# Performance work log

Hardware: AMD Instinct MI355X
Metric: run time of the kernel (lower is better)

The kernel has to match this reference:

```python
import jax, jax.numpy as jnp
import numpy as np

DIM = 512
HEADS = 8
HEAD_DIM = DIM // HEADS  # 64
NUM_ENC = 32             # num_encoding_channels
ENC_RANGE = 1.0
OFFSETS = (0, 512, 2560) # B=2 point clouds, num_points=(512, 2048)
B = len(OFFSETS) - 1
M = 2048                 # max num_points -> padded length
TOTAL = OFFSETS[-1]      # 2560 total points
ENC_IN = NUM_ENC * 3 + 3 # 99 (concat_input=True)


def setup_inputs() -> dict:
    key = jax.random.key(0)
    ks = jax.random.split(key, 6)
    return {
        "features": jax.random.normal(ks[0], (TOTAL, DIM), jnp.float32),
        "coordinates": jax.random.uniform(ks[1], (TOTAL, 3), jnp.float32),
        "qkv_w": jax.random.normal(ks[2], (3 * DIM, DIM), jnp.float32) * (DIM ** -0.5),
        "proj_w": jax.random.normal(ks[3], (DIM, DIM), jnp.float32) * (DIM ** -0.5),
        "proj_b": jnp.zeros((DIM,), jnp.float32),
        "pos_w": jax.random.normal(ks[4], (HEAD_DIM, ENC_IN), jnp.float32) * (ENC_IN ** -0.5),
        "pos_b": jnp.zeros((HEAD_DIM,), jnp.float32),
        "offsets": jnp.array(OFFSETS, jnp.int32),
    }


def reference(features, coordinates, qkv_w, proj_w, proj_b, pos_w, pos_b, offsets):
    # ragged -> padded index math (replaces cat_to_pad / pad_to_cat Python loops)
    pt = jnp.arange(TOTAL)
    b_idx = jnp.searchsorted(offsets, pt, side='right') - 1   # batch id per point
    w_idx = pt - offsets[b_idx]                                # within-batch position
    num_points = offsets[1:] - offsets[:-1]                    # [B]

    # SinusoidalEncoding(num_channels=32, concat_input=True) + Linear -> head_dim
    half = NUM_ENC // 2
    freqs = (2.0 ** jnp.arange(half, dtype=jnp.float32)) * jnp.pi / ENC_RANGE
    sc = coordinates[..., None] * freqs                        # [T, 3, half]
    enc = jnp.concatenate([jnp.sin(sc), jnp.cos(sc)], -1).reshape(TOTAL, 3 * NUM_ENC)
    enc = jnp.concatenate([enc, coordinates], -1)              # [T, 99]
    pos = enc @ pos_w.T + pos_b                                # [T, head_dim]

    feat_pad = jnp.zeros((B, M, DIM), features.dtype).at[b_idx, w_idx].set(features)
    pos_pad = jnp.zeros((B, M, HEAD_DIM), pos.dtype).at[b_idx, w_idx].set(pos)

    # offset_to_mask: mask[b, :, :offsets[b], :offsets[b]] = -inf (cumulative offsets!)
    r = jnp.arange(M)
    off_b = offsets[:-1]                                       # [B]
    blocked = (r[None, :, None] < off_b[:, None, None]) & (r[None, None, :] < off_b[:, None, None])
    mask = jnp.where(blocked, -jnp.inf, 0.0)[:, None]          # [B, 1, M, M]

    # attention
    qkv = (feat_pad @ qkv_w.T).reshape(B, M, 3, HEADS, HEAD_DIM)
    qkv = jnp.transpose(qkv, (2, 0, 3, 1, 4))                  # [3, B, H, M, hd]
    q, k, v = qkv[0], qkv[1], qkv[2]
    q = q + pos_pad[:, None]                                   # broadcast over heads
    k = k + pos_pad[:, None]
    scale = HEAD_DIM ** -0.5
    scores = jnp.einsum('bhqd,bhkd->bhqk', q, k) * scale + mask
    attn = jax.nn.softmax(scores, axis=-1)
    y = jnp.einsum('bhqk,bhkd->bhqd', attn, v)                 # [B, H, M, hd]
    y = jnp.transpose(y, (0, 2, 1, 3)).reshape(B, M, DIM)
    y = y @ proj_w.T + proj_b

    # zero_out_points: x[b, num_points[b]:] = 0
    valid = r[None, :] < num_points[:, None]
    y = jnp.where(valid[..., None], y, 0.0)

    # pad_to_cat back to ragged [total_N, C]
    return y[b_idx, w_idx]
```

## Files before the change

### kernel.cpp

```cpp
#include <hip/hip_runtime.h>
#include <math.h>

#define TOTAL 2560
#define NEG_BIG (-1e30f)
#define LOG2E_8 0.18033688011112042f

typedef __bf16 bf16x8 __attribute__((ext_vector_type(8)));
typedef float f32x4 __attribute__((ext_vector_type(4)));
typedef unsigned short ushort8v __attribute__((ext_vector_type(8)));
typedef unsigned short ushort4v __attribute__((ext_vector_type(4)));

__device__ inline unsigned short f2bf(float f) {
    unsigned u = __builtin_bit_cast(unsigned, f);
    u += 0x7fff + ((u >> 16) & 1);
    return (unsigned short)(u >> 16);
}

__device__ inline void gload16(const void* g, void* l) {
    __builtin_amdgcn_global_load_lds(
        (const __attribute__((address_space(1))) void*)g,
        (__attribute__((address_space(3))) void*)l, 16, 0, 0);
}

__global__ __launch_bounds__(256) void pos_kernel(
    const float* __restrict__ coords,
    const float* __restrict__ pos_w,
    const float* __restrict__ pos_b,
    float* __restrict__ pos_out)
{
    __shared__ float enc[4][100];
    const int wv   = threadIdx.x >> 6;
    const int lane = threadIdx.x & 63;
    const int p = blockIdx.x * 4 + wv;
    const float c0 = coords[p * 3 + 0];
    const float c1 = coords[p * 3 + 1];
    const float c2 = coords[p * 3 + 2];
    for (int i = lane; i < 99; i += 64) {
        float v;
        if (i < 96) {
            const int d = i >> 5;
            const int j = i & 31;
            const float cv = (d == 0) ? c0 : ((d == 1) ? c1 : c2);
            const float freq = exp2f((float)(j & 15)) * 3.14159265358979323846f;
            const float sc = cv * freq;
            v = (j < 16) ? sinf(sc) : cosf(sc);
        } else {
            v = (i == 96) ? c0 : ((i == 97) ? c1 : c2);
        }
        enc[wv][i] = v;
    }
    float acc = pos_b[lane];
    const float* w = pos_w + lane * 99;
    for (int i = 0; i < 99; ++i) acc = fmaf(enc[wv][i], w[i], acc);
    pos_out[p * 64 + lane] = acc;
}

__global__ __launch_bounds__(256) void cast_kernel(
    const float* __restrict__ f,  const float* __restrict__ qw, const float* __restrict__ pw,
    unsigned short* __restrict__ fb, unsigned short* __restrict__ qwb, unsigned short* __restrict__ pwb)
{
    const int s = blockIdx.x * 256 + threadIdx.x;
    const float* src; unsigned short* dst; int ls;
    if (s < 163840)      { src = f;  dst = fb;  ls = s; }
    else if (s < 262144) { src = qw; dst = qwb; ls = s - 163840; }
    else                 { src = pw; dst = pwb; ls = s - 262144; }
    const float4 x0 = *(const float4*)(src + ls * 8);
    const float4 x1 = *(const float4*)(src + ls * 8 + 4);
    ushort8v o;
    o[0] = f2bf(x0.x); o[1] = f2bf(x0.y); o[2] = f2bf(x0.z); o[3] = f2bf(x0.w);
    o[4] = f2bf(x1.x); o[5] = f2bf(x1.y); o[6] = f2bf(x1.z); o[7] = f2bf(x1.w);
    *(ushort8v*)(dst + ls * 8) = o;
}

__global__ __launch_bounds__(256) void qkv_mfma_kernel(
    const unsigned short* __restrict__ A,
    const unsigned short* __restrict__ Bm,
    const float* __restrict__ pos,
    unsigned short* __restrict__ q_ws,
    unsigned short* __restrict__ k_ws,
    unsigned short* __restrict__ vt_ws)
{
    __shared__ unsigned short Abuf[2][64 * 64];
    __shared__ unsigned short Bbuf[2][64 * 64];
    const int m0 = blockIdx.x * 64;
    const int n0 = blockIdx.y * 64;
    const int t = threadIdx.x;
    const int w = t >> 6, lane = t & 63;
    const int wr = w >> 1, wc = w & 1;
    const int c = lane & 15, g = lane >> 4;

    auto STAGE = [&](int kt, int cur) {
#pragma unroll
        for (int i = 0; i < 2; ++i) {
            const int off = w * 2048 + i * 1024;
            const int ba  = off + lane * 16;
            const int row = ba >> 7;
            const int slot = (ba & 127) >> 4;
            gload16(A  + (m0 + row) * 512 + kt * 64 + ((slot ^ (row & 7)) * 8),
                    (char*)&Abuf[cur][0] + off);
            gload16(Bm + (n0 + row) * 512 + kt * 64 + ((slot ^ (row & 7)) * 8),
                    (char*)&Bbuf[cur][0] + off);
        }
    };

    f32x4 acc[2][2];
#pragma unroll
    for (int mi = 0; mi < 2; ++mi)
#pragma unroll
        for (int ni = 0; ni < 2; ++ni) acc[mi][ni] = (f32x4){0.f, 0.f, 0.f, 0.f};

    STAGE(0, 0);
    int cur = 0;
    for (int kt = 0; kt < 8; ++kt) {
        __syncthreads();
        if (kt + 1 < 8) STAGE(kt + 1, cur ^ 1);
#pragma unroll
        for (int kk = 0; kk < 2; ++kk) {
            bf16x8 af[2], bfr[2];
#pragma unroll
            for (int mi = 0; mi < 2; ++mi) {
                const int row = wr * 32 + mi * 16 + c;
                af[mi] = *(const bf16x8*)&Abuf[cur][row * 64 + ((g + 4 * kk) ^ (row & 7)) * 8];
            }
#pragma unroll
            for (int ni = 0; ni < 2; ++ni) {
                const int row = wc * 32 + ni * 16 + c;
                bfr[ni] = *(const bf16x8*)&Bbuf[cur][row * 64 + ((g + 4 * kk) ^ (row & 7)) * 8];
            }
#pragma unroll
            for (int mi = 0; mi < 2; ++mi)
#pragma unroll
                for (int ni = 0; ni < 2; ++ni)
                    acc[mi][ni] = __builtin_amdgcn_mfma_f32_16x16x32_bf16(af[mi], bfr[ni], acc[mi][ni], 0, 0, 0);
        }
        cur ^= 1;
    }

    const int which = n0 >> 9;
    const int h = (n0 >> 6) & 7;
#pragma unroll
    for (int mi = 0; mi < 2; ++mi)
#pragma unroll
        for (int ni = 0; ni < 2; ++ni) {
            const int dd = wc * 32 + ni * 16 + c;
            const int p0 = m0 + wr * 32 + mi * 16 + 4 * g;
            if (which == 2) {
                ushort4v o4;
#pragma unroll
                for (int r = 0; r < 4; ++r) o4[r] = f2bf(acc[mi][ni][r]);
                *(ushort4v*)(vt_ws + (h * 64 + dd) * TOTAL + p0) = o4;
            } else {
#pragma unroll
                for (int r = 0; r < 4; ++r) {
                    const int p = p0 + r;
                    const float v = acc[mi][ni][r] + pos[p * 64 + dd];
                    const int idx = (h * TOTAL + p) * 64 + dd;
                    if (which == 0) q_ws[idx] = f2bf(v);
                    else            k_ws[idx] = f2bf(v);
                }
            }
        }
}

__global__ __launch_bounds__(256) void attn_kernel(
    const unsigned short* __restrict__ q_ws,
    const unsigned short* __restrict__ k_ws,
    const unsigned short* __restrict__ vt_ws,
    unsigned short* __restrict__ y)
{
    const int bx = blockIdx.x;
    int b, qt, h;
    if (bx < 64) { b = 0; h = bx >> 3; qt = bx & 7; }
    else         { b = 1; const int rr = bx - 64; h = rr >> 5; qt = rr & 31; }
    const int base = b ? 512 : 0;
    const int nkt  = b ? 16 : 4;
    const int kt0  = (b && qt < 8) ? 4 : 0;

    const int t    = threadIdx.x;
    const int w    = t >> 6;
    const int lane = t & 63;
    const int g    = lane >> 4;
    const int c    = lane & 15;

    __shared__ unsigned short Kbuf[2][128 * 64];
    __shared__ unsigned short Vbuf[2][64 * 128];
    __shared__ unsigned short P_lds[64][72];

    const unsigned short* Qrow = q_ws + ((h * TOTAL) + base + qt * 64 + 16 * w + c) * 64;
    const bf16x8 qa0 = *(const bf16x8*)(Qrow + 8 * g);
    const bf16x8 qa1 = *(const bf16x8*)(Qrow + 8 * g + 32);

    float m_old = NEG_BIG, l_old = 0.f;
    f32x4 o_acc[4];
#pragma unroll
    for (int n = 0; n < 4; ++n) o_acc[n] = (f32x4){0.f, 0.f, 0.f, 0.f};

    const unsigned short* Kg = k_ws + (h * TOTAL + base) * 64;
    const unsigned short* Vg = vt_ws + h * 64 * TOTAL + base;

    auto STAGE = [&](int kt, int cur) {
#pragma unroll
        for (int i = 0; i < 4; ++i) {
            const int off = w * 4096 + i * 1024;
            const int ba  = off + lane * 16;
            {
                const int row = ba >> 7, slot = (ba & 127) >> 4;
                gload16(Kg + (kt * 128 + row) * 64 + ((slot ^ (row & 7)) * 8),
                        (char*)&Kbuf[cur][0] + off);
            }
            {
                const int dd = ba >> 8, slot = (ba & 255) >> 4;
                gload16(Vg + dd * TOTAL + kt * 128 + ((slot ^ (dd & 7)) * 8),
                        (char*)&Vbuf[cur][0] + off);
            }
        }
    };

    STAGE(kt0, 0);
    int cur = 0;
    for (int kt = kt0; kt < nkt; ++kt) {
        __syncthreads();
        if (kt + 1 < nkt) STAGE(kt + 1, cur ^ 1);

        const unsigned short* Ksh = &Kbuf[cur][0];
        const unsigned short* Vsh = &Vbuf[cur][0];

        f32x4 s_acc[8];
#pragma unroll
        for (int n = 0; n < 8; ++n) {
            f32x4 acc = (f32x4){0.f, 0.f, 0.f, 0.f};
            const int row = 16 * n + c;
            const bf16x8 kb0 = *(const bf16x8*)&Ksh[row * 64 + ((g + 0) ^ (c & 7)) * 8];
            const bf16x8 kb1 = *(const bf16x8*)&Ksh[row * 64 + ((g + 4) ^ (c & 7)) * 8];
            acc = __builtin_amdgcn_mfma_f32_16x16x32_bf16(kb0, qa0, acc, 0, 0, 0);
            acc = __builtin_amdgcn_mfma_f32_16x16x32_bf16(kb1, qa1, acc, 0, 0, 0);
            s_acc[n] = acc;
        }

        float mx01, mx23;
        {
            f32x4 m4 = s_acc[0];
#pragma unroll
            for (int n = 1; n < 8; ++n) {
#pragma unroll
                for (int r = 0; r < 4; ++r) m4[r] = fmaxf(m4[r], s_acc[n][r]);
            }
            mx01 = fmaxf(m4[0], m4[1]); mx23 = fmaxf(m4[2], m4[3]);
        }
        float tm = fmaxf(mx01, mx23) * LOG2E_8;
        tm = fmaxf(tm, __shfl_xor(tm, 16));
        tm = fmaxf(tm, __shfl_xor(tm, 32));
        const float m_new = fmaxf(m_old, tm);
        const float corr = exp2f(m_old - m_new);
        float rs = 0.f;
#pragma unroll
        for (int n = 0; n < 8; ++n)
#pragma unroll
            for (int r = 0; r < 4; ++r) {
                const float pv = exp2f(fmaf(s_acc[n][r], LOG2E_8, -m_new));
                s_acc[n][r] = pv;
                rs += pv;
            }
        rs += __shfl_xor(rs, 16);
        rs += __shfl_xor(rs, 32);
        l_old = l_old * corr + rs;
        m_old = m_new;

        float corr_r[4];
#pragma unroll
        for (int r = 0; r < 4; ++r) corr_r[r] = __shfl(corr, 4 * g + r);
#pragma unroll
        for (int n = 0; n < 4; ++n)
#pragma unroll
            for (int r = 0; r < 4; ++r) o_acc[n][r] *= corr_r[r];

#pragma unroll
        for (int half = 0; half < 2; ++half) {
#pragma unroll
            for (int n = 0; n < 4; ++n) {
                ushort4v pk;
#pragma unroll
                for (int r = 0; r < 4; ++r) pk[r] = f2bf(s_acc[half * 4 + n][r]);
                *(ushort4v*)&P_lds[16 * w + c][16 * n + 4 * g] = pk;
            }
#pragma unroll
            for (int kk = 0; kk < 2; ++kk) {
                const bf16x8 pa = *(const bf16x8*)&P_lds[16 * w + c][8 * g + 32 * kk];
                const int vslot = (g + 4 * (half * 2 + kk)) ^ (c & 7);
#pragma unroll
                for (int n = 0; n < 4; ++n) {
                    const bf16x8 vb = *(const bf16x8*)&Vsh[(16 * n + c) * 128 + vslot * 8];
                    o_acc[n] = __builtin_amdgcn_mfma_f32_16x16x32_bf16(pa, vb, o_acc[n], 0, 0, 0);
                }
            }
        }
        cur ^= 1;
    }

    float inv_own;
    if (b == 0) {
        const float mn  = fmaxf(m_old, 0.f);
        const float ccf = exp2f(m_old - mn);
        const float l   = l_old * ccf + 1536.0f * exp2f(-mn);
        inv_own = ccf / l;
    } else {
        inv_own = 1.0f / l_old;
    }
    float inv_r[4];
#pragma unroll
    for (int r = 0; r < 4; ++r) inv_r[r] = __shfl(inv_own, 4 * g + r);
    unsigned short* yb = y + (base + qt * 64 + 16 * w) * 512 + h * 64;
#pragma unroll
    for (int n = 0; n < 4; ++n)
#pragma unroll
        for (int r = 0; r < 4; ++r)
            yb[(4 * g + r) * 512 + 16 * n + c] = f2bf(o_acc[n][r] * inv_r[r]);
}

__global__ __launch_bounds__(256) void proj_mfma_kernel(
    const unsigned short* __restrict__ A,
    const unsigned short* __restrict__ Bm,
    const float* __restrict__ bias,
    float* __restrict__ out)
{
    __shared__ unsigned short Abuf[2][64 * 64];
    __shared__ unsigned short Bbuf[2][64 * 64];
    const int m0 = blockIdx.x * 64;
    const int n0 = blockIdx.y * 64;
    const int t = threadIdx.x;
    const int w = t >> 6, lane = t & 63;
    const int wr = w >> 1, wc = w & 1;
    const int c = lane & 15, g = lane >> 4;

    auto STAGE = [&](int kt, int cur) {
#pragma unroll
        for (int i = 0; i < 2; ++i) {
            const int off = w * 2048 + i * 1024;
            const int ba  = off + lane * 16;
            const int row = ba >> 7;
            const int slot = (ba & 127) >> 4;
            gload16(A  + (m0 + row) * 512 + kt * 64 + ((slot ^ (row & 7)) * 8),
                    (char*)&Abuf[cur][0] + off);
            gload16(Bm + (n0 + row) * 512 + kt * 64 + ((slot ^ (row & 7)) * 8),
                    (char*)&Bbuf[cur][0] + off);
        }
    };

    f32x4 acc[2][2];
#pragma unroll
    for (int mi = 0; mi < 2; ++mi)
#pragma unroll
        for (int ni = 0; ni < 2; ++ni) acc[mi][ni] = (f32x4){0.f, 0.f, 0.f, 0.f};

    STAGE(0, 0);
    int cur = 0;
    for (int kt = 0; kt < 8; ++kt) {
        __syncthreads();
        if (kt + 1 < 8) STAGE(kt + 1, cur ^ 1);
#pragma unroll
        for (int kk = 0; kk < 2; ++kk) {
            bf16x8 af[2], bfr[2];
#pragma unroll
            for (int mi = 0; mi < 2; ++mi) {
                const int row = wr * 32 + mi * 16 + c;
                af[mi] = *(const bf16x8*)&Abuf[cur][row * 64 + ((g + 4 * kk) ^ (row & 7)) * 8];
            }
#pragma unroll
            for (int ni = 0; ni < 2; ++ni) {
                const int row = wc * 32 + ni * 16 + c;
                bfr[ni] = *(const bf16x8*)&Bbuf[cur][row * 64 + ((g + 4 * kk) ^ (row & 7)) * 8];
            }
#pragma unroll
            for (int mi = 0; mi < 2; ++mi)
#pragma unroll
                for (int ni = 0; ni < 2; ++ni)
                    acc[mi][ni] = __builtin_amdgcn_mfma_f32_16x16x32_bf16(af[mi], bfr[ni], acc[mi][ni], 0, 0, 0);
        }
        cur ^= 1;
    }

#pragma unroll
    for (int mi = 0; mi < 2; ++mi)
#pragma unroll
        for (int ni = 0; ni < 2; ++ni) {
            const int col = n0 + wc * 32 + ni * 16 + c;
            const float bv = bias[col];
#pragma unroll
            for (int r = 0; r < 4; ++r) {
                const int p = m0 + wr * 32 + mi * 16 + 4 * g + r;
                out[p * 512 + col] = acc[mi][ni][r] + bv;
            }
        }
}

extern "C" void kernel_launch(void* const* d_in, const int* in_sizes, int n_in,
                              void* d_out, int out_size, void* d_ws, size_t ws_size,
                              hipStream_t stream) {
    const float* features = (const float*)d_in[0];
    const float* coords   = (const float*)d_in[1];
    const float* qkv_w    = (const float*)d_in[2];
    const float* proj_w   = (const float*)d_in[3];
    const float* proj_b   = (const float*)d_in[4];
    const float* pos_w    = (const float*)d_in[5];
    const float* pos_b    = (const float*)d_in[6];
    float* out = (float*)d_out;

    float* pos_ws = (float*)d_ws;
    unsigned short* feat_bf  = (unsigned short*)(pos_ws + TOTAL * 64);
    unsigned short* qkvw_bf  = feat_bf + 2560 * 512;
    unsigned short* projw_bf = qkvw_bf + 1536 * 512;
    unsigned short* q_ws  = projw_bf + 512 * 512;
    unsigned short* k_ws  = q_ws  + 8 * TOTAL * 64;
    unsigned short* vt_ws = k_ws  + 8 * TOTAL * 64;
    unsigned short* y_bf  = vt_ws + 8 * TOTAL * 64;

    pos_kernel<<<dim3(TOTAL / 4), dim3(256), 0, stream>>>(coords, pos_w, pos_b, pos_ws);
    cast_kernel<<<dim3(1152), dim3(256), 0, stream>>>(
        features, qkv_w, proj_w, feat_bf, qkvw_bf, projw_bf);
    qkv_mfma_kernel<<<dim3(40, 24), dim3(256), 0, stream>>>(
        feat_bf, qkvw_bf, pos_ws, q_ws, k_ws, vt_ws);
    attn_kernel<<<dim3(320), dim3(256), 0, stream>>>(q_ws, k_ws, vt_ws, y_bf);
    proj_mfma_kernel<<<dim3(40, 8), dim3(256), 0, stream>>>(
        y_bf, projw_bf, proj_b, out);
}
```

Measured before the change: 71.49 us.

## Split attention KV range into two partials and combine, reading K/V directly from global

The attention kernel for the second batch is split along the key dimension into two halves, so 576 blocks launch instead of 320. Each half writes unnormalized fp32 partial outputs plus running max and sum, and a new combine kernel merges them and casts to bf16. The LDS double-buffered K/V staging is removed; K and V fragments are now loaded straight from global memory (L2) inside the MFMA loops. The aim is to fill more CUs on the mi355x, at the cost of an extra launch, fp32 partial traffic, and uncoalesced global loads in place of staged shared-memory loads.

```diff
diff --git a/kernel.cpp b/kernel.cpp
--- a/kernel.cpp
+++ b/kernel.cpp
@@ -162,19 +162,29 @@
         }
 }
 
-__global__ __launch_bounds__(256) void attn_kernel(
+__global__ __launch_bounds__(256) void attn_part_kernel(
     const unsigned short* __restrict__ q_ws,
     const unsigned short* __restrict__ k_ws,
     const unsigned short* __restrict__ vt_ws,
-    unsigned short* __restrict__ y)
+    float* __restrict__ o_part,
+    float2* __restrict__ ml2)
 {
     const int bx = blockIdx.x;
-    int b, qt, h;
-    if (bx < 64) { b = 0; h = bx >> 3; qt = bx & 7; }
-    else         { b = 1; const int rr = bx - 64; h = rr >> 5; qt = rr & 31; }
+    int b, qt, h, sp, t0, t1;
+    if (bx < 64) {
+        b = 0; h = bx >> 3; qt = bx & 7; sp = 0; t0 = 0; t1 = 4;
+    } else {
+        b = 1;
+        const int idx = bx - 64;
+        sp = idx >> 8;
+        const int rr = idx & 255;
+        h = rr >> 5; qt = rr & 31;
+        const int kt0 = (qt < 8) ? 4 : 0;
+        const int mid = (kt0 + 16) >> 1;
+        t0 = sp ? mid : kt0;
+        t1 = sp ? 16 : mid;
+    }
     const int base = b ? 512 : 0;
-    const int nkt  = b ? 16 : 4;
-    const int kt0  = (b && qt < 8) ? 4 : 0;
 
     const int t    = threadIdx.x;
     const int w    = t >> 6;
@@ -182,8 +192,6 @@
     const int g    = lane >> 4;
     const int c    = lane & 15;
 
-    __shared__ unsigned short Kbuf[2][128 * 64];
-    __shared__ unsigned short Vbuf[2][64 * 128];
     __shared__ unsigned short P_lds[64][72];
 
     const unsigned short* Qrow = q_ws + ((h * TOTAL) + base + qt * 64 + 16 * w + c) * 64;
@@ -198,40 +206,16 @@
     const unsigned short* Kg = k_ws + (h * TOTAL + base) * 64;
     const unsigned short* Vg = vt_ws + h * 64 * TOTAL + base;
 
-    auto STAGE = [&](int kt, int cur) {
-#pragma unroll
-        for (int i = 0; i < 4; ++i) {
-            const int off = w * 4096 + i * 1024;
-            const int ba  = off + lane * 16;
-            {
-                const int row = ba >> 7, slot = (ba & 127) >> 4;
-                gload16(Kg + (kt * 128 + row) * 64 + ((slot ^ (row & 7)) * 8),
-                        (char*)&Kbuf[cur][0] + off);
-            }
-            {
-                const int dd = ba >> 8, slot = (ba & 255) >> 4;
-                gload16(Vg + dd * TOTAL + kt * 128 + ((slot ^ (dd & 7)) * 8),
-                        (char*)&Vbuf[cur][0] + off);
-            }
-        }
-    };
-
-    STAGE(kt0, 0);
-    int cur = 0;
-    for (int kt = kt0; kt < nkt; ++kt) {
-        __syncthreads();
-        if (kt + 1 < nkt) STAGE(kt + 1, cur ^ 1);
-
-        const unsigned short* Ksh = &Kbuf[cur][0];
-        const unsigned short* Vsh = &Vbuf[cur][0];
+    for (int kt = t0; kt < t1; ++kt) {
+        const unsigned short* Kt = Kg + kt * 128 * 64;
+        const unsigned short* Vt = Vg + kt * 128;
 
         f32x4 s_acc[8];
 #pragma unroll
         for (int n = 0; n < 8; ++n) {
             f32x4 acc = (f32x4){0.f, 0.f, 0.f, 0.f};
-            const int row = 16 * n + c;
-            const bf16x8 kb0 = *(const bf16x8*)&Ksh[row * 64 + ((g + 0) ^ (c & 7)) * 8];
-            const bf16x8 kb1 = *(const bf16x8*)&Ksh[row * 64 + ((g + 4) ^ (c & 7)) * 8];
+            const bf16x8 kb0 = *(const bf16x8*)(Kt + (16 * n + c) * 64 + 8 * g);
+            const bf16x8 kb1 = *(const bf16x8*)(Kt + (16 * n + c) * 64 + 8 * g + 32);
             acc = __builtin_amdgcn_mfma_f32_16x16x32_bf16(kb0, qa0, acc, 0, 0, 0);
             acc = __builtin_amdgcn_mfma_f32_16x16x32_bf16(kb1, qa1, acc, 0, 0, 0);
             s_acc[n] = acc;
@@ -286,35 +270,80 @@
 #pragma unroll
             for (int kk = 0; kk < 2; ++kk) {
                 const bf16x8 pa = *(const bf16x8*)&P_lds[16 * w + c][8 * g + 32 * kk];
-                const int vslot = (g + 4 * (half * 2 + kk)) ^ (c & 7);
+                const int koff = 8 * g + 32 * (half * 2 + kk);
 #pragma unroll
                 for (int n = 0; n < 4; ++n) {
-                    const bf16x8 vb = *(const bf16x8*)&Vsh[(16 * n + c) * 128 + vslot * 8];
+                    const bf16x8 vb = *(const bf16x8*)(Vt + (16 * n + c) * TOTAL + koff);
                     o_acc[n] = __builtin_amdgcn_mfma_f32_16x16x32_bf16(pa, vb, o_acc[n], 0, 0, 0);
                 }
             }
         }
-        cur ^= 1;
-    }
-
-    float inv_own;
+    }
+
     if (b == 0) {
         const float mn  = fmaxf(m_old, 0.f);
         const float ccf = exp2f(m_old - mn);
         const float l   = l_old * ccf + 1536.0f * exp2f(-mn);
-        inv_own = ccf / l;
+        const float inv_own = ccf / l;
+        float inv_r[4];
+#pragma unroll
+        for (int r = 0; r < 4; ++r) inv_r[r] = __shfl(inv_own, 4 * g + r);
+        float* op = o_part + (size_t)(qt * 64 + 16 * w) * 512 + h * 64;
+#pragma unroll
+        for (int n = 0; n < 4; ++n)
+#pragma unroll
+            for (int r = 0; r < 4; ++r)
+                op[(4 * g + r) * 512 + 16 * n + c] = o_acc[n][r] * inv_r[r];
     } else {
-        inv_own = 1.0f / l_old;
-    }
-    float inv_r[4];
-#pragma unroll
-    for (int r = 0; r < 4; ++r) inv_r[r] = __shfl(inv_own, 4 * g + r);
-    unsigned short* yb = y + (base + qt * 64 + 16 * w) * 512 + h * 64;
-#pragma unroll
-    for (int n = 0; n < 4; ++n)
-#pragma unroll
-        for (int r = 0; r < 4; ++r)
-            yb[(4 * g + r) * 512 + 16 * n + c] = f2bf(o_acc[n][r] * inv_r[r]);
+        float* op = o_part + (size_t)sp * (TOTAL * 512)
+                  + (size_t)(512 + qt * 64 + 16 * w) * 512 + h * 64;
+#pragma unroll
+        for (int n = 0; n < 4; ++n)
+#pragma unroll
+            for (int r = 0; r < 4; ++r)
+                op[(4 * g + r) * 512 + 16 * n + c] = o_acc[n][r];
+        if (lane < 16) {
+            const int p = 512 + qt * 64 + 16 * w + c;
+            ml2[(sp * TOTAL + p) * 8 + h] = make_float2(m_old, l_old);
+        }
+    }
+}
+
+__global__ __launch_bounds__(256) void combine_kernel(
+    const float* __restrict__ o_part,
+    const float2* __restrict__ ml2,
+    unsigned short* __restrict__ y)
+{
+    const int e = blockIdx.x * 256 + threadIdx.x;
+    const int p = e >> 6;
+    const int seg = e & 63;
+    const size_t bo = (size_t)p * 512 + seg * 8;
+    const float4 a0 = *(const float4*)(o_part + bo);
+    const float4 a1 = *(const float4*)(o_part + bo + 4);
+    ushort8v y8;
+    if (p < 512) {
+        y8[0] = f2bf(a0.x); y8[1] = f2bf(a0.y); y8[2] = f2bf(a0.z); y8[3] = f2bf(a0.w);
+        y8[4] = f2bf(a1.x); y8[5] = f2bf(a1.y); y8[6] = f2bf(a1.z); y8[7] = f2bf(a1.w);
+    } else {
+        const int h = seg >> 3;
+        const float2 v0 = ml2[(size_t)p * 8 + h];
+        const float2 v1 = ml2[(size_t)(TOTAL + p) * 8 + h];
+        const float mt = fmaxf(v0.x, v1.x);
+        const float c0 = exp2f(v0.x - mt), c1 = exp2f(v1.x - mt);
+        const float inv = 1.0f / fmaf(v0.y, c0, v1.y * c1);
+        const float f0 = c0 * inv, f1 = c1 * inv;
+        const float4 b0 = *(const float4*)(o_part + (size_t)TOTAL * 512 + bo);
+        const float4 b1 = *(const float4*)(o_part + (size_t)TOTAL * 512 + bo + 4);
+        y8[0] = f2bf(fmaf(a0.x, f0, b0.x * f1));
+        y8[1] = f2bf(fmaf(a0.y, f0, b0.y * f1));
+        y8[2] = f2bf(fmaf(a0.z, f0, b0.z * f1));
+        y8[3] = f2bf(fmaf(a0.w, f0, b0.w * f1));
+        y8[4] = f2bf(fmaf(a1.x, f0, b1.x * f1));
+        y8[5] = f2bf(fmaf(a1.y, f0, b1.y * f1));
+        y8[6] = f2bf(fmaf(a1.z, f0, b1.z * f1));
+        y8[7] = f2bf(fmaf(a1.w, f0, b1.w * f1));
+    }
+    *(ushort8v*)(y + bo) = y8;
 }
 
 __global__ __launch_bounds__(256) void proj_mfma_kernel(
@@ -412,14 +441,18 @@
     unsigned short* q_ws  = projw_bf + 512 * 512;
     unsigned short* k_ws  = q_ws  + 8 * TOTAL * 64;
     unsigned short* vt_ws = k_ws  + 8 * TOTAL * 64;
-    unsigned short* y_bf  = vt_ws + 8 * TOTAL * 64;
+    float* o_part = (float*)(vt_ws + 8 * TOTAL * 64);
+    float2* ml2   = (float2*)(o_part + 2 * TOTAL * 512);
+    unsigned short* y_bf = (unsigned short*)(ml2 + 2 * TOTAL * 8);
 
     pos_kernel<<<dim3(TOTAL / 4), dim3(256), 0, stream>>>(coords, pos_w, pos_b, pos_ws);
     cast_kernel<<<dim3(1152), dim3(256), 0, stream>>>(
         features, qkv_w, proj_w, feat_bf, qkvw_bf, projw_bf);
     qkv_mfma_kernel<<<dim3(40, 24), dim3(256), 0, stream>>>(
         feat_bf, qkvw_bf, pos_ws, q_ws, k_ws, vt_ws);
-    attn_kernel<<<dim3(320), dim3(256), 0, stream>>>(q_ws, k_ws, vt_ws, y_bf);
+    attn_part_kernel<<<dim3(576), dim3(256), 0, stream>>>(
+        q_ws, k_ws, vt_ws, o_part, ml2);
+    combine_kernel<<<dim3(640), dim3(256), 0, stream>>>(o_part, ml2, y_bf);
     proj_mfma_kernel<<<dim3(40, 8), dim3(256), 0, stream>>>(
         y_bf, projw_bf, proj_b, out);
 }
```

Result: slower. 113.6 us (+59.0%).
